# Performance work log

Hardware: AMD Instinct MI355X
Metric: run time of the kernel (lower is better)

## Reference

```python
import jax, jax.numpy as jnp
import numpy as np

B, N = 2, 256
RC = 6.0
BOX = 12.0
# (center_radius, eta) for G2; kappas for G3; (eta, zeta, lambda) for G4/G5
G2_PARAMS = [(rs, eta) for rs in (0.0, 2.0) for eta in (0.1, 1.0)]
G3_KAPPAS = [1.0, 2.0]
G45_PARAMS = [(eta, zeta, lam) for eta in (0.01, 0.1) for zeta in (1.0, 4.0) for lam in (-1.0, 1.0)]


def _fc(r, rc):
    # Behler cosine cutoff: 0.5*(cos(pi r / rc) + 1) for r < rc, else 0
    return 0.5 * (jnp.cos(jnp.pi * r / rc) + 1.0) * (r < rc)


def setup_inputs() -> dict:
    key = jax.random.key(0)
    k1, k2 = jax.random.split(key)
    atomic_numbers = jax.random.randint(k1, (N,), 1, 10).astype(jnp.float32)
    coordinates = jax.random.uniform(k2, (B, N, 3), dtype=jnp.float32) * BOX
    return {"atomic_numbers": atomic_numbers, "coordinates": coordinates}


def reference(atomic_numbers, coordinates):
    b, n, _ = coordinates.shape
    # r_ij vector = x_i - x_j, matching coords.unsqueeze(-2) - coords.unsqueeze(-3)
    dvec = coordinates[:, :, None, :] - coordinates[:, None, :, :]        # [B,N,N,3]
    sq = jnp.sum(dvec * dvec, axis=-1)                                    # [B,N,N]
    pair_mask = ~jnp.eye(n, dtype=bool)                                   # j != i
    sq_safe = jnp.where(pair_mask, sq, 1.0)
    r = jnp.where(pair_mask, jnp.sqrt(sq_safe), 0.0)                      # [B,N,N]
    fcr = _fc(r, RC) * pair_mask                                          # cutoff, self excluded

    feats = [jnp.broadcast_to(atomic_numbers, (b, n))]
    # G1: sum_j fc(r_ij)
    feats.append(jnp.sum(fcr, axis=-1))
    # G2: sum_j exp(-eta*(r_ij - Rs)^2) * fc(r_ij)
    for rs, eta in G2_PARAMS:
        feats.append(jnp.sum(jnp.exp(-eta * (r - rs) ** 2) * fcr, axis=-1))
    # G3: sum_j cos(kappa * r_ij) * fc(r_ij)
    for kappa in G3_KAPPAS:
        feats.append(jnp.sum(jnp.cos(kappa * r) * fcr, axis=-1))

    # shared angular (triplet) quantities, each [B,N,N,N]
    dot = jnp.einsum('bijc,bikc->bijk', dvec, dvec)
    denom = r[:, :, :, None] * r[:, :, None, :]
    cos_t = dot / jnp.where(denom > 0, denom, 1.0)
    sq_ij = sq[:, :, :, None]
    sq_ik = sq[:, :, None, :]
    sq_jk = sq[:, None, :, :]
    sq3 = sq_ij + sq_ik + sq_jk
    sq2 = sq_ij + sq_ik
    # fc products: fcr already zero on the diagonal, so fc3 vanishes whenever
    # j==i, k==i, or j==k (full triplet mask for G4)
    fc3 = fcr[:, :, :, None] * fcr[:, :, None, :] * fcr[:, None, :, :]
    fc2 = fcr[:, :, :, None] * fcr[:, :, None, :] * pair_mask[None, None, :, :]

    # G4: 2^(1-zeta) sum_{j!=k} (1+lam*cos)^zeta exp(-eta*(rij^2+rik^2+rjk^2)) fc fc fc
    for eta, zeta, lam in G45_PARAMS:
        ang = jnp.maximum(1.0 + lam * cos_t, 0.0) ** zeta
        feats.append((2.0 ** (1.0 - zeta)) * jnp.sum(ang * jnp.exp(-eta * sq3) * fc3, axis=(-2, -1)))
    # G5: 2^(1-zeta) sum_{j!=k} (1+lam*cos)^zeta exp(-eta*(rij^2+rik^2)) fc fc
    for eta, zeta, lam in G45_PARAMS:
        ang = jnp.maximum(1.0 + lam * cos_t, 0.0) ** zeta
        feats.append((2.0 ** (1.0 - zeta)) * jnp.sum(ang * jnp.exp(-eta * sq2) * fc2, axis=(-2, -1)))

    return jnp.stack(feats, axis=-1)  # [B, N, 24]
```

## Files before the change

kernel.cpp:

```cpp
#include <hip/hip_runtime.h>
#include <math.h>

#define NN 256
#define NF 24
#define NFEAT 23
#define RCUT 6.0f
#define PI_F 3.14159265358979323846f
#define NSEG 8

__device__ __forceinline__ void pair_body(const float4 gj, const float4 wj,
                                          const float4 g, const float4 w,
                                          float* acc)
{
    const float ddx = gj.x - g.x, ddy = gj.y - g.y, ddz = gj.z - g.z;
    const float sqjk = ddx * ddx + ddy * ddy + ddz * ddz;
    const float rjk = sqrtf(sqjk);
    const float fcjk = (rjk < RCUT) ? 0.5f * (__cosf((PI_F / RCUT) * rjk) + 1.0f) : 0.0f;
    const float dot = gj.x * g.x + gj.y * g.y + gj.z * g.z;
    const float cost = dot * gj.w * g.w;
    const float base = wj.x * w.x;
    const float f3 = base * fcjk;
    const float e2a = wj.y * w.y;
    const float e2b = wj.z * w.z;
    const float e3a = e2a * __expf(-0.01f * sqjk);
    const float e3b = e2b * __expf(-0.1f * sqjk);
    const float c1m = fmaxf(1.0f - cost, 0.0f);
    const float c1p = fmaxf(1.0f + cost, 0.0f);
    const float c2m = c1m * c1m, c2p = c1p * c1p;
    const float c4m = c2m * c2m, c4p = c2p * c2p;
    const float w3a = e3a * f3, w3b = e3b * f3;
    const float w2a = e2a * base, w2b = e2b * base;
    acc[7]  += c1m * w3a;  acc[8]  += c1p * w3a;
    acc[9]  += c4m * w3a;  acc[10] += c4p * w3a;
    acc[11] += c1m * w3b;  acc[12] += c1p * w3b;
    acc[13] += c4m * w3b;  acc[14] += c4p * w3b;
    acc[15] += c1m * w2a;  acc[16] += c1p * w2a;
    acc[17] += c4m * w2a;  acc[18] += c4p * w2a;
    acc[19] += c1m * w2b;  acc[20] += c1p * w2b;
    acc[21] += c4m * w2b;  acc[22] += c4p * w2b;
}

__global__ __launch_bounds__(64) void feat_kernel(
    const float* __restrict__ coords,
    float* __restrict__ ws)
{
    const int i    = blockIdx.x;
    const int b    = blockIdx.y;
    const int seg  = blockIdx.z;
    const int lane = threadIdx.x;

    __shared__ float4 geo[NN];
    __shared__ float4 wgt[NN];
    __shared__ float red[NFEAT];

    const float* cb = coords + (size_t)b * NN * 3;
    const float xi = cb[i * 3 + 0], yi = cb[i * 3 + 1], zi = cb[i * 3 + 2];

    float acc[NFEAT];
#pragma unroll
    for (int t = 0; t < NFEAT; t++) acc[t] = 0.0f;

    int m = 0;
#pragma unroll
    for (int rnd = 0; rnd < 4; ++rnd) {
        const int j = lane + (rnd << 6);
        const float xj = cb[j * 3 + 0], yj = cb[j * 3 + 1], zj = cb[j * 3 + 2];
        const float dx = xi - xj, dy = yi - yj, dz = zi - zj;
        const float r2 = dx * dx + dy * dy + dz * dz;
        const float r  = sqrtf(r2);
        const bool incut = (j != i) && (r < RCUT);
        const float fc = incut ? 0.5f * (__cosf((PI_F / RCUT) * r) + 1.0f) : 0.0f;
        if (seg == 0) {
            acc[0] += fc;
            acc[1] += __expf(-0.1f * r2) * fc;
            acc[2] += __expf(-1.0f * r2) * fc;
            const float d = r - 2.0f;
            acc[3] += __expf(-0.1f * d * d) * fc;
            acc[4] += __expf(-1.0f * d * d) * fc;
            acc[5] += __cosf(r) * fc;
            acc[6] += __cosf(2.0f * r) * fc;
        }
        const unsigned long long bal = __ballot(incut);
        if (incut) {
            const int p = m + __popcll(bal & ((1ULL << lane) - 1ULL));
            geo[p] = make_float4(dx, dy, dz, 1.0f / r);
            wgt[p] = make_float4(fc, __expf(-0.01f * r2), __expf(-0.1f * r2), 0.0f);
        }
        m += __popcll(bal);
    }
    __syncthreads();

    if (m >= 2) {
        const int Rfull = (m - 1) >> 1;
        const int tlo = 1 + (Rfull * seg) / NSEG;
        const int thi = (Rfull * (seg + 1)) / NSEG;
        const bool halfseg = (seg == NSEG - 1) && ((m & 1) == 0);
        const int mh = m >> 1;
        for (int rnd = 0; rnd < 4; ++rnd) {
            const int jj = lane + (rnd << 6);
            if (jj >= m) break;
            const float4 gj = geo[jj];
            const float4 wj = wgt[jj];
            for (int t = tlo; t <= thi; ++t) {
                int kk = jj + t; if (kk >= m) kk -= m;
                pair_body(gj, wj, geo[kk], wgt[kk], acc);
            }
            if (halfseg && jj < mh)
                pair_body(gj, wj, geo[jj + mh], wgt[jj + mh], acc);
        }
    }

#pragma unroll
    for (int t = 0; t < NFEAT; t++) {
        float v = acc[t];
        for (int off = 32; off > 0; off >>= 1)
            v += __shfl_down(v, off, 64);
        if (lane == 0) red[t] = v;
    }
    __syncthreads();
    if (lane < NFEAT)
        ws[(((size_t)b * NN + i) * NSEG + seg) * NFEAT + lane] = red[lane];
}

__global__ __launch_bounds__(256) void reduce_kernel(
    const float* __restrict__ Z,
    const float* __restrict__ ws,
    float* __restrict__ out)
{
    const int idx = blockIdx.x * 256 + threadIdx.x;
    const int f  = idx % NF;
    const int ai = idx / NF;
    if (f == 0) { out[idx] = Z[ai & (NN - 1)]; return; }
    float v = 0.0f;
    const float* p = ws + ((size_t)ai * NSEG) * NFEAT + (f - 1);
#pragma unroll
    for (int s = 0; s < NSEG; ++s) v += p[s * NFEAT];
    if (f >= 8) {
        const int a = (f - 8) & 3;
        v *= (a >= 2) ? 0.25f : 2.0f;
    }
    out[idx] = v;
}

extern "C" void kernel_launch(void* const* d_in, const int* in_sizes, int n_in,
                              void* d_out, int out_size, void* d_ws, size_t ws_size,
                              hipStream_t stream) {
    const float* Z = (const float*)d_in[0];
    const float* coords = (const float*)d_in[1];
    float* out = (float*)d_out;
    float* ws = (float*)d_ws;
    dim3 grid(NN, 2, NSEG);
    feat_kernel<<<grid, dim3(64), 0, stream>>>(coords, ws);
    const int total = 2 * NN * NF;
    reduce_kernel<<<total / 256, 256, 0, stream>>>(Z, ws, out);
}
```

Baseline: 72.92 us.

## Split neighbor compaction into setup kernel and widen triplet work split

```diff
diff --git a/kernel.cpp b/kernel.cpp
--- a/kernel.cpp
+++ b/kernel.cpp
@@ -3,62 +3,32 @@
 
 #define NN 256
 #define NF 24
-#define NFEAT 23
 #define RCUT 6.0f
 #define PI_F 3.14159265358979323846f
-#define NSEG 8
+#define NSEG 16
 
-__device__ __forceinline__ void pair_body(const float4 gj, const float4 wj,
-                                          const float4 g, const float4 w,
-                                          float* acc)
+#define GEO_OFF  (4096)
+#define WGT_OFF  (4096 + 2*1024*1024)
+#define PART_OFF (4096 + 4*1024*1024)
+
+__global__ __launch_bounds__(64) void setup_kernel(
+    const float* __restrict__ Z,
+    const float* __restrict__ coords,
+    float* __restrict__ out,
+    void* __restrict__ wsv)
 {
-    const float ddx = gj.x - g.x, ddy = gj.y - g.y, ddz = gj.z - g.z;
-    const float sqjk = ddx * ddx + ddy * ddy + ddz * ddz;
-    const float rjk = sqrtf(sqjk);
-    const float fcjk = (rjk < RCUT) ? 0.5f * (__cosf((PI_F / RCUT) * rjk) + 1.0f) : 0.0f;
-    const float dot = gj.x * g.x + gj.y * g.y + gj.z * g.z;
-    const float cost = dot * gj.w * g.w;
-    const float base = wj.x * w.x;
-    const float f3 = base * fcjk;
-    const float e2a = wj.y * w.y;
-    const float e2b = wj.z * w.z;
-    const float e3a = e2a * __expf(-0.01f * sqjk);
-    const float e3b = e2b * __expf(-0.1f * sqjk);
-    const float c1m = fmaxf(1.0f - cost, 0.0f);
-    const float c1p = fmaxf(1.0f + cost, 0.0f);
-    const float c2m = c1m * c1m, c2p = c1p * c1p;
-    const float c4m = c2m * c2m, c4p = c2p * c2p;
-    const float w3a = e3a * f3, w3b = e3b * f3;
-    const float w2a = e2a * base, w2b = e2b * base;
-    acc[7]  += c1m * w3a;  acc[8]  += c1p * w3a;
-    acc[9]  += c4m * w3a;  acc[10] += c4p * w3a;
-    acc[11] += c1m * w3b;  acc[12] += c1p * w3b;
-    acc[13] += c4m * w3b;  acc[14] += c4p * w3b;
-    acc[15] += c1m * w2a;  acc[16] += c1p * w2a;
-    acc[17] += c4m * w2a;  acc[18] += c4p * w2a;
-    acc[19] += c1m * w2b;  acc[20] += c1p * w2b;
-    acc[21] += c4m * w2b;  acc[22] += c4p * w2b;
-}
-
-__global__ __launch_bounds__(64) void feat_kernel(
-    const float* __restrict__ coords,
-    float* __restrict__ ws)
-{
-    const int i    = blockIdx.x;
-    const int b    = blockIdx.y;
-    const int seg  = blockIdx.z;
-    const int lane = threadIdx.x;
-
-    __shared__ float4 geo[NN];
-    __shared__ float4 wgt[NN];
-    __shared__ float red[NFEAT];
+    const int i = blockIdx.x, b = blockIdx.y, lane = threadIdx.x;
+    const int ai = b * NN + i;
+    int* m_arr = (int*)wsv;
+    float4* geoC = (float4*)((char*)wsv + GEO_OFF) + (size_t)ai * NN;
+    float4* wgtC = (float4*)((char*)wsv + WGT_OFF) + (size_t)ai * NN;
 
     const float* cb = coords + (size_t)b * NN * 3;
     const float xi = cb[i * 3 + 0], yi = cb[i * 3 + 1], zi = cb[i * 3 + 2];
 
-    float acc[NFEAT];
+    float acc[7];
 #pragma unroll
-    for (int t = 0; t < NFEAT; t++) acc[t] = 0.0f;
+    for (int t = 0; t < 7; t++) acc[t] = 0.0f;
 
     int m = 0;
 #pragma unroll
@@ -70,25 +40,65 @@
         const float r  = sqrtf(r2);
         const bool incut = (j != i) && (r < RCUT);
         const float fc = incut ? 0.5f * (__cosf((PI_F / RCUT) * r) + 1.0f) : 0.0f;
-        if (seg == 0) {
-            acc[0] += fc;
-            acc[1] += __expf(-0.1f * r2) * fc;
-            acc[2] += __expf(-1.0f * r2) * fc;
-            const float d = r - 2.0f;
-            acc[3] += __expf(-0.1f * d * d) * fc;
-            acc[4] += __expf(-1.0f * d * d) * fc;
-            acc[5] += __cosf(r) * fc;
-            acc[6] += __cosf(2.0f * r) * fc;
-        }
+        acc[0] += fc;
+        acc[1] += __expf(-0.1f * r2) * fc;
+        acc[2] += __expf(-1.0f * r2) * fc;
+        const float d = r - 2.0f;
+        acc[3] += __expf(-0.1f * d * d) * fc;
+        acc[4] += __expf(-1.0f * d * d) * fc;
+        acc[5] += __cosf(r) * fc;
+        acc[6] += __cosf(2.0f * r) * fc;
         const unsigned long long bal = __ballot(incut);
         if (incut) {
             const int p = m + __popcll(bal & ((1ULL << lane) - 1ULL));
-            geo[p] = make_float4(dx, dy, dz, 1.0f / r);
-            wgt[p] = make_float4(fc, __expf(-0.01f * r2), __expf(-0.1f * r2), 0.0f);
+            geoC[p] = make_float4(dx, dy, dz, 1.0f / r);
+            wgtC[p] = make_float4(fc, __expf(-0.01f * r2), __expf(-0.1f * r2), 0.0f);
         }
         m += __popcll(bal);
     }
+    if (lane == 0) m_arr[ai] = m;
+
+#pragma unroll
+    for (int t = 0; t < 7; t++) {
+        float v = acc[t];
+        for (int off = 32; off > 0; off >>= 1) v += __shfl_down(v, off, 64);
+        acc[t] = v;
+    }
+    if (lane == 0) {
+        float* ob = out + (size_t)ai * NF;
+        ob[0] = Z[i];
+#pragma unroll
+        for (int t = 0; t < 7; t++) ob[1 + t] = acc[t];
+    }
+}
+
+__global__ __launch_bounds__(256) void pair_kernel(
+    const void* __restrict__ wsv_in, void* __restrict__ wsv_out)
+{
+    const int i = blockIdx.x, b = blockIdx.y;
+    const int tid = threadIdx.x, lane = tid & 63, wave = tid >> 6;
+    const int seg = blockIdx.z * 4 + wave;
+    const int ai = b * NN + i;
+
+    const int* m_arr = (const int*)wsv_in;
+    const float4* geoC = (const float4*)((const char*)wsv_in + GEO_OFF) + (size_t)ai * NN;
+    const float4* wgtC = (const float4*)((const char*)wsv_in + WGT_OFF) + (size_t)ai * NN;
+    float* part = (float*)((char*)wsv_out + PART_OFF);
+
+    __shared__ float4 geo[NN];
+    __shared__ float4 wgt[NN];
+    __shared__ float red[4][16];
+
+    const int m = m_arr[ai];
+    for (int idx = tid; idx < m; idx += 256) {
+        geo[idx] = geoC[idx];
+        wgt[idx] = wgtC[idx];
+    }
     __syncthreads();
+
+    float acc[16];
+#pragma unroll
+    for (int t = 0; t < 16; t++) acc[t] = 0.0f;
 
     if (m >= 2) {
         const int Rfull = (m - 1) >> 1;
@@ -101,45 +111,66 @@
             if (jj >= m) break;
             const float4 gj = geo[jj];
             const float4 wj = wgt[jj];
-            for (int t = tlo; t <= thi; ++t) {
-                int kk = jj + t; if (kk >= m) kk -= m;
-                pair_body(gj, wj, geo[kk], wgt[kk], acc);
+            for (int t = tlo; t <= thi + (halfseg && jj < mh ? 1 : 0); ++t) {
+                int kk = jj + ((t > thi) ? mh : t); if (kk >= m) kk -= m;
+                const float4 g = geo[kk];
+                const float4 w = wgt[kk];
+                const float ddx = gj.x - g.x, ddy = gj.y - g.y, ddz = gj.z - g.z;
+                const float sqjk = ddx * ddx + ddy * ddy + ddz * ddz;
+                const float rjk = sqrtf(sqjk);
+                const float fcjk = (rjk < RCUT) ? 0.5f * (__cosf((PI_F / RCUT) * rjk) + 1.0f) : 0.0f;
+                const float dot = gj.x * g.x + gj.y * g.y + gj.z * g.z;
+                const float cost = dot * gj.w * g.w;
+                const float base = wj.x * w.x;
+                const float f3 = base * fcjk;
+                const float e2a = wj.y * w.y;
+                const float e2b = wj.z * w.z;
+                const float e3a = e2a * __expf(-0.01f * sqjk);
+                const float e3b = e2b * __expf(-0.1f * sqjk);
+                const float c1m = fmaxf(1.0f - cost, 0.0f);
+                const float c1p = fmaxf(1.0f + cost, 0.0f);
+                const float c2m = c1m * c1m, c2p = c1p * c1p;
+                const float c4m = c2m * c2m, c4p = c2p * c2p;
+                const float w3a = e3a * f3, w3b = e3b * f3;
+                const float w2a = e2a * base, w2b = e2b * base;
+                acc[0]  += c1m * w3a;  acc[1]  += c1p * w3a;
+                acc[2]  += c4m * w3a;  acc[3]  += c4p * w3a;
+                acc[4]  += c1m * w3b;  acc[5]  += c1p * w3b;
+                acc[6]  += c4m * w3b;  acc[7]  += c4p * w3b;
+                acc[8]  += c1m * w2a;  acc[9]  += c1p * w2a;
+                acc[10] += c4m * w2a;  acc[11] += c4p * w2a;
+                acc[12] += c1m * w2b;  acc[13] += c1p * w2b;
+                acc[14] += c4m * w2b;  acc[15] += c4p * w2b;
             }
-            if (halfseg && jj < mh)
-                pair_body(gj, wj, geo[jj + mh], wgt[jj + mh], acc);
         }
     }
 
 #pragma unroll
-    for (int t = 0; t < NFEAT; t++) {
+    for (int t = 0; t < 16; t++) {
         float v = acc[t];
-        for (int off = 32; off > 0; off >>= 1)
-            v += __shfl_down(v, off, 64);
-        if (lane == 0) red[t] = v;
+        for (int off = 32; off > 0; off >>= 1) v += __shfl_down(v, off, 64);
+        if (lane == 0) red[wave][t] = v;
     }
     __syncthreads();
-    if (lane < NFEAT)
-        ws[(((size_t)b * NN + i) * NSEG + seg) * NFEAT + lane] = red[lane];
+    if (tid < 64) {
+        const int w2 = tid >> 4, f = tid & 15;
+        part[((size_t)ai * NSEG + (blockIdx.z * 4 + w2)) * 16 + f] = red[w2][f];
+    }
 }
 
 __global__ __launch_bounds__(256) void reduce_kernel(
-    const float* __restrict__ Z,
-    const float* __restrict__ ws,
-    float* __restrict__ out)
+    const void* __restrict__ wsv, float* __restrict__ out)
 {
     const int idx = blockIdx.x * 256 + threadIdx.x;
-    const int f  = idx % NF;
-    const int ai = idx / NF;
-    if (f == 0) { out[idx] = Z[ai & (NN - 1)]; return; }
+    const int f  = idx & 15;
+    const int ai = idx >> 4;
+    const float* p = (const float*)((const char*)wsv + PART_OFF)
+                   + ((size_t)ai * NSEG) * 16 + f;
     float v = 0.0f;
-    const float* p = ws + ((size_t)ai * NSEG) * NFEAT + (f - 1);
 #pragma unroll
-    for (int s = 0; s < NSEG; ++s) v += p[s * NFEAT];
-    if (f >= 8) {
-        const int a = (f - 8) & 3;
-        v *= (a >= 2) ? 0.25f : 2.0f;
-    }
-    out[idx] = v;
+    for (int s = 0; s < NSEG; ++s) v += p[s * 16];
+    v *= ((f & 3) >= 2) ? 0.25f : 2.0f;
+    out[(size_t)ai * NF + 8 + f] = v;
 }
 
 extern "C" void kernel_launch(void* const* d_in, const int* in_sizes, int n_in,
@@ -148,9 +179,7 @@
     const float* Z = (const float*)d_in[0];
     const float* coords = (const float*)d_in[1];
     float* out = (float*)d_out;
-    float* ws = (float*)d_ws;
-    dim3 grid(NN, 2, NSEG);
-    feat_kernel<<<grid, dim3(64), 0, stream>>>(coords, ws);
-    const int total = 2 * NN * NF;
-    reduce_kernel<<<total / 256, 256, 0, stream>>>(Z, ws, out);
+    setup_kernel<<<dim3(NN, 2), dim3(64), 0, stream>>>(Z, coords, out, d_ws);
+    pair_kernel<<<dim3(NN, 2, NSEG / 4), dim3(256), 0, stream>>>(d_ws, d_ws);
+    reduce_kernel<<<dim3(2 * NN * 16 / 256), dim3(256), 0, stream>>>(d_ws, out);
 }
```

After: 75.16 us. 1.03x slower.
